# Performance work log

Measured on AMD Instinct MI355X. Metric: run time of the kernel, lower is better.

Reference implementation:

```python
import jax, jax.numpy as jnp
import numpy as np

EPS = 1e-12  # torch F.normalize eps


def setup_inputs() -> dict:
    key = jax.random.key(0)
    k1, k2, k3 = jax.random.split(key, 3)
    b, c, n, h, w = 8, 64, 8, 64, 64
    dims = 32
    x = jax.random.normal(k1, (b, c, n, h, w), dtype=jnp.float32)
    # 1x1 conv kernels collapse to [out_ch, in_ch] matrices
    w_q = jax.random.normal(k2, (dims, c), dtype=jnp.float32) * (1.0 / np.sqrt(c))
    w_kv = jax.random.normal(k3, (2 * dims, c), dtype=jnp.float32) * (1.0 / np.sqrt(c))
    return {"x": x, "w_q": w_q, "w_kv": w_kv}


def _l2norm(t, axis):
    nrm = jnp.sqrt(jnp.sum(t * t, axis=axis, keepdims=True))
    return t / jnp.maximum(nrm, EPS)


def reference(x, w_q, w_kv):
    b, c, n, h, w = x.shape
    d = w_q.shape[0]
    # spa_q: 1x1 stride-1 conv == channel GEMM -> [b, d, n, h, w]
    q = jnp.einsum('bcnhw,dc->bdnhw', x, w_q)
    x_s = x[:, :, :, ::2, ::2]                       # [b, c, n, h2, w2]
    kv = jnp.einsum('bcnhw,ec->benhw', x_s, w_kv)    # [b, 2d, n, h2, w2]
    k, v = kv[:, :d], kv[:, d:]
    h2, w2 = k.shape[-2], k.shape[-1]
    # unfold_q: b (h w) (d n)
    uq = q.transpose(0, 3, 4, 1, 2).reshape(b, h * w, d * n)
    # unfold_k: b (d n) (h2 w2)
    uk = k.reshape(b, d * n, h2 * w2)
    # unfold_v: b (h2 w2) (d n)
    uv = v.transpose(0, 3, 4, 1, 2).reshape(b, h2 * w2, d * n)
    uq = _l2norm(uq, axis=-1)
    uk = _l2norm(uk, axis=-2)
    att = jax.nn.softmax(jnp.einsum('bqf,bfk->bqk', uq, uk), axis=-1)
    out = jnp.einsum('bqk,bkf->bqf', att, uv)        # [b, h*w, d*n]
    # b (h w) (d n) -> b d n h w
    return out.reshape(b, h, w, d, n).transpose(0, 3, 4, 1, 2)
```

## Files before the change

kernel.cpp:

```cpp
#include <hip/hip_runtime.h>


typedef __attribute__((ext_vector_type(8))) short short8;
typedef __attribute__((ext_vector_type(4))) float floatx4;
typedef __attribute__((ext_vector_type(2))) unsigned uintx2;

__device__ __forceinline__ short f2bf(float f) {
    unsigned u = __builtin_bit_cast(unsigned, f);
    u += 0x7fffu + ((u >> 16) & 1u);
    return (short)(u >> 16);
}
__device__ __forceinline__ unsigned pack2bf(float a, float b) {
    return (unsigned)(unsigned short)f2bf(a) | ((unsigned)(unsigned short)f2bf(b) << 16);
}

__global__ __launch_bounds__(256) void proj(const float* __restrict__ x,
                                            const float* __restrict__ wq,
                                            const float* __restrict__ wkv,
                                            short* __restrict__ qraw,
                                            short* __restrict__ kraw,
                                            short* __restrict__ vraw) {
    int b = blockIdx.x >> 6, y = blockIdx.x & 63;
    int t = threadIdx.x;
    int n = t >> 5, dg = (t >> 3) & 3, xc = t & 7;
    bool kv = (y & 1) == 0;
    int y2 = y >> 1;

    __shared__ __align__(16) float wq_s[64 * 32];
    __shared__ __align__(16) float wkv_s[64 * 64];
    __shared__ __align__(16) float xs[128 * 36];
    __shared__ __align__(16) short k_lds[16 * 264];
    __shared__ __align__(16) short v_lds[256 * 16];
    __shared__ float red[32 * 33];
    __shared__ float nrm[32];
    short* q_lds = (short*)xs;

    for (int i = t; i < 2048; i += 256) { int d = i >> 6, c = i & 63; wq_s[c * 32 + d] = wq[i]; }
    for (int i = t; i < 4096; i += 256) { int e = i >> 6, c = i & 63; wkv_s[c * 64 + e] = wkv[i]; }
    const float* xb = x + (size_t)b * 2097152 + y * 64;

    for (int xh = 0; xh < 2; ++xh) {
        float qa[8][4], ka[8][2], va[8][2];
#pragma unroll
        for (int j = 0; j < 8; ++j) {
            qa[j][0] = qa[j][1] = qa[j][2] = qa[j][3] = 0.f;
            ka[j][0] = ka[j][1] = 0.f; va[j][0] = va[j][1] = 0.f;
        }
        for (int cc = 0; cc < 4; ++cc) {
            __syncthreads();
#pragma unroll
            for (int it = 0; it < 4; ++it) {
                int i = it * 256 + t, cn = i >> 3, e = i & 7;
                float4 v = *(const float4*)(xb + (size_t)(cc * 16 + (cn >> 3)) * 32768 + (cn & 7) * 4096 + xh * 32 + e * 4);
                *(float4*)(xs + cn * 36 + e * 4) = v;
            }
            __syncthreads();
            for (int c = 0; c < 16; ++c) {
                float4 xv = *(const float4*)(xs + (c * 8 + n) * 36 + xc * 4);
                float xw[4] = {xv.x, xv.y, xv.z, xv.w};
                int cg = cc * 16 + c;
                float4 wqa = *(const float4*)(wq_s + cg * 32 + dg * 8);
                float4 wqb = *(const float4*)(wq_s + cg * 32 + dg * 8 + 4);
                float wj[8] = {wqa.x, wqa.y, wqa.z, wqa.w, wqb.x, wqb.y, wqb.z, wqb.w};
#pragma unroll
                for (int j = 0; j < 8; ++j)
#pragma unroll
                    for (int i2 = 0; i2 < 4; ++i2) qa[j][i2] += wj[j] * xw[i2];
                if (kv) {
                    float4 wka = *(const float4*)(wkv_s + cg * 64 + dg * 8);
                    float4 wkb = *(const float4*)(wkv_s + cg * 64 + dg * 8 + 4);
                    float4 wva = *(const float4*)(wkv_s + cg * 64 + 32 + dg * 8);
                    float4 wvb = *(const float4*)(wkv_s + cg * 64 + 32 + dg * 8 + 4);
                    float wk[8] = {wka.x, wka.y, wka.z, wka.w, wkb.x, wkb.y, wkb.z, wkb.w};
                    float wv2[8] = {wva.x, wva.y, wva.z, wva.w, wvb.x, wvb.y, wvb.z, wvb.w};
#pragma unroll
                    for (int j = 0; j < 8; ++j) {
                        ka[j][0] += wk[j] * xw[0]; ka[j][1] += wk[j] * xw[2];
                        va[j][0] += wv2[j] * xw[0]; va[j][1] += wv2[j] * xw[2];
                    }
                }
            }
        }
        __syncthreads();
#pragma unroll
        for (int i2 = 0; i2 < 4; ++i2) {
            float s = 0.f;
#pragma unroll
            for (int j = 0; j < 8; ++j) s += qa[j][i2] * qa[j][i2];
            red[(xc * 4 + i2) * 33 + n * 4 + dg] = s;
        }
        __syncthreads();
        if (t < 32) {
            float s = 0.f;
            for (int k = 0; k < 32; ++k) s += red[t * 33 + k];
            nrm[t] = 1.f / fmaxf(sqrtf(s), 1e-12f);
        }
        __syncthreads();
#pragma unroll
        for (int i2 = 0; i2 < 4; ++i2) {
            float sc = nrm[xc * 4 + i2];
#pragma unroll
            for (int j = 0; j < 8; ++j)
                q_lds[(xc * 4 + i2) * 264 + (dg * 8 + j) * 8 + n] = f2bf(qa[j][i2] * sc);
        }
        __syncthreads();
        {
            size_t qg = ((size_t)b * 4096 + y * 64 + xh * 32) * 256;
#pragma unroll
            for (int it = 0; it < 4; ++it) {
                int r = it * 8 + (t >> 5), sg = t & 31;
                *(uint4*)(qraw + qg + (size_t)r * 256 + sg * 8) = *(const uint4*)(q_lds + r * 264 + sg * 8);
            }
        }
        if (kv) {
            __syncthreads();
#pragma unroll
            for (int ii = 0; ii < 2; ++ii) {
                float s = 0.f;
#pragma unroll
                for (int j = 0; j < 8; ++j) s += ka[j][ii] * ka[j][ii];
                red[(xc * 2 + ii) * 33 + n * 4 + dg] = s;
            }
            __syncthreads();
            if (t < 16) {
                float s = 0.f;
                for (int k = 0; k < 32; ++k) s += red[t * 33 + k];
                nrm[t] = 1.f / fmaxf(sqrtf(s), 1e-12f);
            }
            __syncthreads();
#pragma unroll
            for (int ii = 0; ii < 2; ++ii) {
                float sc = nrm[xc * 2 + ii];
#pragma unroll
                for (int j = 0; j < 8; ++j) {
                    int f = (dg * 8 + j) * 8 + n;
                    k_lds[(xc * 2 + ii) * 264 + f] = f2bf(ka[j][ii] * sc);
                    v_lds[f * 16 + xc * 2 + ii] = f2bf(va[j][ii]);
                }
            }
            __syncthreads();
            size_t kg = ((size_t)b * 1024 + y2 * 32 + xh * 16) * 256;
#pragma unroll
            for (int it = 0; it < 2; ++it) {
                int r = it * 8 + (t >> 5), sg = t & 31;
                *(uint4*)(kraw + kg + (size_t)r * 256 + sg * 8) = *(const uint4*)(k_lds + r * 264 + sg * 8);
            }
            size_t vg = (size_t)b * 262144 + (size_t)y2 * 32 + xh * 16;
#pragma unroll
            for (int it = 0; it < 2; ++it) {
                int idx = it * 256 + t, f = idx >> 1, hh = idx & 1;
                *(uint4*)(vraw + vg + (size_t)f * 1024 + hh * 8) = *(const uint4*)(v_lds + f * 16 + hh * 8);
            }
        }
    }
}

__global__ __launch_bounds__(256, 1) void attn(const short* __restrict__ qraw,
                                               const short* __restrict__ kraw,
                                               const short* __restrict__ vraw,
                                               float* __restrict__ out) {
    int b = blockIdx.x >> 5, qt = blockIdx.x & 31;
    int t = threadIdx.x, wv = t >> 6, lane = t & 63, l16 = lane & 15, quad = lane >> 4;

    __shared__ __align__(16) short k_s[2][32 * 264];
    __shared__ __align__(16) short v_s[2][256 * 40];
    __shared__ __align__(16) short p_s[2][128 * 40];
    __shared__ float dsum[128];

    short8 qf[2][8];
    const short* qb = qraw + ((size_t)b * 4096 + qt * 128 + wv * 32) * 256;
#pragma unroll
    for (int pt = 0; pt < 2; ++pt)
#pragma unroll
        for (int fs = 0; fs < 8; ++fs)
            qf[pt][fs] = *(const short8*)(qb + (pt * 16 + l16) * 256 + fs * 32 + quad * 8);

    floatx4 acc[8][4];
#pragma unroll
    for (int i = 0; i < 8; ++i)
#pragma unroll
        for (int j = 0; j < 4; ++j) acc[i][j] = (floatx4){0.f, 0.f, 0.f, 0.f};
    float dacc0 = 0.f, dacc1 = 0.f;

    int krow = t >> 3, kseg = t & 7;
    const short* kbase = kraw + ((size_t)b * 1024 + krow) * 256 + kseg * 32;
    const short* vbase = vraw + ((size_t)b * 256 + t) * 1024;

    short8 kst[4], vst[4];
#pragma unroll
    for (int j = 0; j < 4; ++j) {
        kst[j] = *(const short8*)(kbase + j * 8);
        vst[j] = *(const short8*)(vbase + j * 8);
    }
#pragma unroll
    for (int j = 0; j < 4; ++j) {
        *(short8*)(k_s[0] + krow * 264 + kseg * 32 + j * 8) = kst[j];
        *(short8*)(v_s[0] + t * 40 + j * 8) = vst[j];
    }
#pragma unroll
    for (int j = 0; j < 4; ++j) {
        kst[j] = *(const short8*)(kbase + (size_t)32 * 256 + j * 8);
        vst[j] = *(const short8*)(vbase + 32 + j * 8);
    }
    __syncthreads();

    for (int kc = 0; kc < 32; ++kc) {
        int cur = kc & 1, nxt = cur ^ 1;
        floatx4 cc0[2] = {(floatx4){0.f,0.f,0.f,0.f}, (floatx4){0.f,0.f,0.f,0.f}};
        floatx4 cc1[2] = {(floatx4){0.f,0.f,0.f,0.f}, (floatx4){0.f,0.f,0.f,0.f}};
#pragma unroll
        for (int kt = 0; kt < 2; ++kt) {
#pragma unroll
            for (int fs = 0; fs < 8; ++fs) {
                short8 a = *(const short8*)(k_s[cur] + (kt * 16 + l16) * 264 + fs * 32 + quad * 8);
                cc0[kt] = __builtin_amdgcn_mfma_f32_16x16x32_bf16(a, qf[0][fs], cc0[kt], 0, 0, 0);
                cc1[kt] = __builtin_amdgcn_mfma_f32_16x16x32_bf16(a, qf[1][fs], cc1[kt], 0, 0, 0);
            }
        }
#pragma unroll
        for (int kt = 0; kt < 2; ++kt) {
            float e0 = __expf(cc0[kt][0]), e1 = __expf(cc0[kt][1]);
            float e2 = __expf(cc0[kt][2]), e3 = __expf(cc0[kt][3]);
            dacc0 += (e0 + e1) + (e2 + e3);
            uintx2 w0; w0[0] = pack2bf(e0, e1); w0[1] = pack2bf(e2, e3);
            *(uintx2*)(p_s[cur] + (wv * 32 + l16) * 40 + kt * 16 + quad * 4) = w0;
            float f0 = __expf(cc1[kt][0]), f1 = __expf(cc1[kt][1]);
            float f2 = __expf(cc1[kt][2]), f3 = __expf(cc1[kt][3]);
            dacc1 += (f0 + f1) + (f2 + f3);
            uintx2 w1; w1[0] = pack2bf(f0, f1); w1[1] = pack2bf(f2, f3);
            *(uintx2*)(p_s[cur] + (wv * 32 + 16 + l16) * 40 + kt * 16 + quad * 4) = w1;
        }
        __syncthreads();

        if (kc < 31) {
#pragma unroll
            for (int j = 0; j < 4; ++j) {
                *(short8*)(k_s[nxt] + krow * 264 + kseg * 32 + j * 8) = kst[j];
                *(short8*)(v_s[nxt] + t * 40 + j * 8) = vst[j];
            }
        }
        short8 av[4];
#pragma unroll
        for (int fl = 0; fl < 4; ++fl)
            av[fl] = *(const short8*)(v_s[cur] + (wv * 64 + fl * 16 + l16) * 40 + quad * 8);
#pragma unroll
        for (int p2 = 0; p2 < 8; ++p2) {
            short8 bq = *(const short8*)(p_s[cur] + (p2 * 16 + l16) * 40 + quad * 8);
#pragma unroll
            for (int fl = 0; fl < 4; ++fl)
                acc[p2][fl] = __builtin_amdgcn_mfma_f32_16x16x32_bf16(av[fl], bq, acc[p2][fl], 0, 0, 0);
        }
        if (kc < 30) {
            int kp0n = (kc + 2) * 32;
#pragma unroll
            for (int j = 0; j < 4; ++j) {
                kst[j] = *(const short8*)(kbase + (size_t)kp0n * 256 + j * 8);
                vst[j] = *(const short8*)(vbase + kp0n + j * 8);
            }
        }
        __syncthreads();
    }
    dacc0 += __shfl_xor(dacc0, 16); dacc0 += __shfl_xor(dacc0, 32);
    dacc1 += __shfl_xor(dacc1, 16); dacc1 += __shfl_xor(dacc1, 32);
    if (quad == 0) {
        dsum[wv * 32 + l16] = dacc0;
        dsum[wv * 32 + 16 + l16] = dacc1;
    }
    __syncthreads();
    float* ob = out + (size_t)b * 1048576 + qt * 128;
#pragma unroll
    for (int p2 = 0; p2 < 8; ++p2) {
        float inv = 1.f / dsum[p2 * 16 + l16];
#pragma unroll
        for (int fl = 0; fl < 4; ++fl) {
            int f0 = wv * 64 + fl * 16 + quad * 4;
#pragma unroll
            for (int r = 0; r < 4; ++r)
                ob[(size_t)(f0 + r) * 4096 + p2 * 16 + l16] = acc[p2][fl][r] * inv;
        }
    }
}

extern "C" void kernel_launch(void* const* d_in, const int* in_sizes, int n_in,
                              void* d_out, int out_size, void* d_ws, size_t ws_size,
                              hipStream_t stream) {
    (void)in_sizes; (void)n_in; (void)out_size; (void)ws_size;
    const float* x   = (const float*)d_in[0];
    const float* wqp = (const float*)d_in[1];
    const float* wkv = (const float*)d_in[2];
    float* out = (float*)d_out;

    char* ws = (char*)d_ws;
    short* qraw = (short*)ws;
    short* kraw = (short*)(ws + 16777216);
    short* vraw = (short*)(ws + 16777216 + 4194304);

    proj<<<512, 256, 0, stream>>>(x, wqp, wkv, qraw, kraw, vraw);
    attn<<<256, 256, 0, stream>>>(qraw, kraw, vraw, out);
}
```

Measured before the change: 194.7 us.

## Split attention block across 8 waves with swizzled LDS and hardware bf16 pack

Doubles the attention block to 512 threads. The S=QK^T work is split by key half and the PV work is split by feature and query halves, so each wave holds half the accumulators. The two per-key-half denominator partials are combined at the end. K/V LDS stores and reads get an XOR swizzle to cut bank conflicts, the software bf16 rounding is replaced by v_cvt_pk_bf16_f32, and s_setprio is raised around MFMA loops. The aim is more waves per CU to hide latency and lower register pressure, at the cost of duplicated Q fragment loads and more threads per barrier.

```diff
diff --git a/kernel.cpp b/kernel.cpp
--- a/kernel.cpp
+++ b/kernel.cpp
@@ -10,8 +10,11 @@
     u += 0x7fffu + ((u >> 16) & 1u);
     return (short)(u >> 16);
 }
-__device__ __forceinline__ unsigned pack2bf(float a, float b) {
-    return (unsigned)(unsigned short)f2bf(a) | ((unsigned)(unsigned short)f2bf(b) << 16);
+
+__device__ __forceinline__ unsigned cvtpk_bf16(float lo, float hi) {
+    unsigned r;
+    asm("v_cvt_pk_bf16_f32 %0, %1, %2" : "=v"(r) : "v"(lo), "v"(hi));
+    return r;
 }
 
 __global__ __launch_bounds__(256) void proj(const float* __restrict__ x,
@@ -155,7 +158,7 @@
     }
 }
 
-__global__ __launch_bounds__(256, 1) void attn(const short* __restrict__ qraw,
+__global__ __launch_bounds__(512, 2) void attn(const short* __restrict__ qraw,
                                                const short* __restrict__ kraw,
                                                const short* __restrict__ vraw,
                                                float* __restrict__ out) {
@@ -165,97 +168,104 @@
     __shared__ __align__(16) short k_s[2][32 * 264];
     __shared__ __align__(16) short v_s[2][256 * 40];
     __shared__ __align__(16) short p_s[2][128 * 40];
-    __shared__ float dsum[128];
+    __shared__ float dsum[2][128];
+
+    int kt = wv & 1, pp = wv >> 1;
+    int fh = wv & 3, ph = wv >> 2;
 
     short8 qf[2][8];
-    const short* qb = qraw + ((size_t)b * 4096 + qt * 128 + wv * 32) * 256;
+    const short* qb = qraw + ((size_t)b * 4096 + qt * 128 + pp * 32) * 256;
 #pragma unroll
     for (int pt = 0; pt < 2; ++pt)
 #pragma unroll
         for (int fs = 0; fs < 8; ++fs)
             qf[pt][fs] = *(const short8*)(qb + (pt * 16 + l16) * 256 + fs * 32 + quad * 8);
 
-    floatx4 acc[8][4];
-#pragma unroll
-    for (int i = 0; i < 8; ++i)
+    floatx4 acc[4][4];
+#pragma unroll
+    for (int i = 0; i < 4; ++i)
 #pragma unroll
         for (int j = 0; j < 4; ++j) acc[i][j] = (floatx4){0.f, 0.f, 0.f, 0.f};
     float dacc0 = 0.f, dacc1 = 0.f;
 
-    int krow = t >> 3, kseg = t & 7;
-    const short* kbase = kraw + ((size_t)b * 1024 + krow) * 256 + kseg * 32;
-    const short* vbase = vraw + ((size_t)b * 256 + t) * 1024;
-
-    short8 kst[4], vst[4];
-#pragma unroll
-    for (int j = 0; j < 4; ++j) {
+    int krow = t >> 4, kseg = t & 15;
+    int vrow = t >> 1, vhalf = t & 1;
+    int sk = (kseg >> 2) & 1, sv = (t >> 4) & 1;
+    const short* kbase = kraw + ((size_t)b * 1024 + krow) * 256 + kseg * 16;
+    const short* vbase = vraw + ((size_t)b * 256 + vrow) * 1024 + vhalf * 16;
+
+    short8 kst[2], vst[2];
+#pragma unroll
+    for (int j = 0; j < 2; ++j) {
         kst[j] = *(const short8*)(kbase + j * 8);
         vst[j] = *(const short8*)(vbase + j * 8);
     }
 #pragma unroll
-    for (int j = 0; j < 4; ++j) {
-        *(short8*)(k_s[0] + krow * 264 + kseg * 32 + j * 8) = kst[j];
-        *(short8*)(v_s[0] + t * 40 + j * 8) = vst[j];
-    }
-#pragma unroll
-    for (int j = 0; j < 4; ++j) {
-        kst[j] = *(const short8*)(kbase + (size_t)32 * 256 + j * 8);
+    for (int j = 0; j < 2; ++j) {
+        *(short8*)(k_s[0] + krow * 264 + kseg * 16 + (j ^ sk) * 8) = kst[j];
+        *(short8*)(v_s[0] + vrow * 40 + vhalf * 16 + (j ^ sv) * 8) = vst[j];
+    }
+#pragma unroll
+    for (int j = 0; j < 2; ++j) {
+        kst[j] = *(const short8*)(kbase + 8192 + j * 8);
         vst[j] = *(const short8*)(vbase + 32 + j * 8);
     }
     __syncthreads();
 
+    int s2 = (l16 >> 3) & 1;
     for (int kc = 0; kc < 32; ++kc) {
         int cur = kc & 1, nxt = cur ^ 1;
-        floatx4 cc0[2] = {(floatx4){0.f,0.f,0.f,0.f}, (floatx4){0.f,0.f,0.f,0.f}};
-        floatx4 cc1[2] = {(floatx4){0.f,0.f,0.f,0.f}, (floatx4){0.f,0.f,0.f,0.f}};
-#pragma unroll
-        for (int kt = 0; kt < 2; ++kt) {
-#pragma unroll
-            for (int fs = 0; fs < 8; ++fs) {
-                short8 a = *(const short8*)(k_s[cur] + (kt * 16 + l16) * 264 + fs * 32 + quad * 8);
-                cc0[kt] = __builtin_amdgcn_mfma_f32_16x16x32_bf16(a, qf[0][fs], cc0[kt], 0, 0, 0);
-                cc1[kt] = __builtin_amdgcn_mfma_f32_16x16x32_bf16(a, qf[1][fs], cc1[kt], 0, 0, 0);
-            }
-        }
-#pragma unroll
-        for (int kt = 0; kt < 2; ++kt) {
-            float e0 = __expf(cc0[kt][0]), e1 = __expf(cc0[kt][1]);
-            float e2 = __expf(cc0[kt][2]), e3 = __expf(cc0[kt][3]);
+        floatx4 cc0 = (floatx4){0.f, 0.f, 0.f, 0.f};
+        floatx4 cc1 = (floatx4){0.f, 0.f, 0.f, 0.f};
+        const short* krd = k_s[cur] + (kt * 16 + l16) * 264;
+        __builtin_amdgcn_s_setprio(1);
+#pragma unroll
+        for (int fs = 0; fs < 8; ++fs) {
+            short8 a = *(const short8*)(krd + fs * 32 + (quad ^ ((fs >> 1) & 1)) * 8);
+            cc0 = __builtin_amdgcn_mfma_f32_16x16x32_bf16(a, qf[0][fs], cc0, 0, 0, 0);
+            cc1 = __builtin_amdgcn_mfma_f32_16x16x32_bf16(a, qf[1][fs], cc1, 0, 0, 0);
+        }
+        __builtin_amdgcn_s_setprio(0);
+        {
+            float e0 = __expf(cc0[0]), e1 = __expf(cc0[1]);
+            float e2 = __expf(cc0[2]), e3 = __expf(cc0[3]);
             dacc0 += (e0 + e1) + (e2 + e3);
-            uintx2 w0; w0[0] = pack2bf(e0, e1); w0[1] = pack2bf(e2, e3);
-            *(uintx2*)(p_s[cur] + (wv * 32 + l16) * 40 + kt * 16 + quad * 4) = w0;
-            float f0 = __expf(cc1[kt][0]), f1 = __expf(cc1[kt][1]);
-            float f2 = __expf(cc1[kt][2]), f3 = __expf(cc1[kt][3]);
+            uintx2 w0; w0[0] = cvtpk_bf16(e0, e1); w0[1] = cvtpk_bf16(e2, e3);
+            *(uintx2*)(p_s[cur] + (pp * 32 + l16) * 40 + kt * 16 + quad * 4) = w0;
+            float f0 = __expf(cc1[0]), f1 = __expf(cc1[1]);
+            float f2 = __expf(cc1[2]), f3 = __expf(cc1[3]);
             dacc1 += (f0 + f1) + (f2 + f3);
-            uintx2 w1; w1[0] = pack2bf(f0, f1); w1[1] = pack2bf(f2, f3);
-            *(uintx2*)(p_s[cur] + (wv * 32 + 16 + l16) * 40 + kt * 16 + quad * 4) = w1;
+            uintx2 w1; w1[0] = cvtpk_bf16(f0, f1); w1[1] = cvtpk_bf16(f2, f3);
+            *(uintx2*)(p_s[cur] + (pp * 32 + 16 + l16) * 40 + kt * 16 + quad * 4) = w1;
         }
         __syncthreads();
 
         if (kc < 31) {
 #pragma unroll
-            for (int j = 0; j < 4; ++j) {
-                *(short8*)(k_s[nxt] + krow * 264 + kseg * 32 + j * 8) = kst[j];
-                *(short8*)(v_s[nxt] + t * 40 + j * 8) = vst[j];
+            for (int j = 0; j < 2; ++j) {
+                *(short8*)(k_s[nxt] + krow * 264 + kseg * 16 + (j ^ sk) * 8) = kst[j];
+                *(short8*)(v_s[nxt] + vrow * 40 + vhalf * 16 + (j ^ sv) * 8) = vst[j];
             }
         }
         short8 av[4];
 #pragma unroll
         for (int fl = 0; fl < 4; ++fl)
-            av[fl] = *(const short8*)(v_s[cur] + (wv * 64 + fl * 16 + l16) * 40 + quad * 8);
-#pragma unroll
-        for (int p2 = 0; p2 < 8; ++p2) {
-            short8 bq = *(const short8*)(p_s[cur] + (p2 * 16 + l16) * 40 + quad * 8);
+            av[fl] = *(const short8*)(v_s[cur] + (fh * 64 + fl * 16 + l16) * 40 + (quad ^ s2) * 8);
+        __builtin_amdgcn_s_setprio(1);
+#pragma unroll
+        for (int p2 = 0; p2 < 4; ++p2) {
+            short8 bq = *(const short8*)(p_s[cur] + (ph * 64 + p2 * 16 + l16) * 40 + quad * 8);
 #pragma unroll
             for (int fl = 0; fl < 4; ++fl)
                 acc[p2][fl] = __builtin_amdgcn_mfma_f32_16x16x32_bf16(av[fl], bq, acc[p2][fl], 0, 0, 0);
         }
+        __builtin_amdgcn_s_setprio(0);
         if (kc < 30) {
-            int kp0n = (kc + 2) * 32;
-#pragma unroll
-            for (int j = 0; j < 4; ++j) {
-                kst[j] = *(const short8*)(kbase + (size_t)kp0n * 256 + j * 8);
-                vst[j] = *(const short8*)(vbase + kp0n + j * 8);
+            int koff = (kc + 2) * 8192, voff = (kc + 2) * 32;
+#pragma unroll
+            for (int j = 0; j < 2; ++j) {
+                kst[j] = *(const short8*)(kbase + koff + j * 8);
+                vst[j] = *(const short8*)(vbase + voff + j * 8);
             }
         }
         __syncthreads();
@@ -263,20 +273,21 @@
     dacc0 += __shfl_xor(dacc0, 16); dacc0 += __shfl_xor(dacc0, 32);
     dacc1 += __shfl_xor(dacc1, 16); dacc1 += __shfl_xor(dacc1, 32);
     if (quad == 0) {
-        dsum[wv * 32 + l16] = dacc0;
-        dsum[wv * 32 + 16 + l16] = dacc1;
+        dsum[kt][pp * 32 + l16] = dacc0;
+        dsum[kt][pp * 32 + 16 + l16] = dacc1;
     }
     __syncthreads();
     float* ob = out + (size_t)b * 1048576 + qt * 128;
 #pragma unroll
-    for (int p2 = 0; p2 < 8; ++p2) {
-        float inv = 1.f / dsum[p2 * 16 + l16];
+    for (int p2 = 0; p2 < 4; ++p2) {
+        int pcol = ph * 64 + p2 * 16 + l16;
+        float inv = 1.f / (dsum[0][pcol] + dsum[1][pcol]);
 #pragma unroll
         for (int fl = 0; fl < 4; ++fl) {
-            int f0 = wv * 64 + fl * 16 + quad * 4;
+            int f0 = fh * 64 + fl * 16 + quad * 4;
 #pragma unroll
             for (int r = 0; r < 4; ++r)
-                ob[(size_t)(f0 + r) * 4096 + p2 * 16 + l16] = acc[p2][fl][r] * inv;
+                ob[(size_t)(f0 + r) * 4096 + pcol] = acc[p2][fl][r] * inv;
         }
     }
 }
@@ -296,5 +307,5 @@
     short* vraw = (short*)(ws + 16777216 + 4194304);
 
     proj<<<512, 256, 0, stream>>>(x, wqp, wkv, qraw, kraw, vraw);
-    attn<<<256, 256, 0, stream>>>(qraw, kraw, vraw, out);
-}
+    attn<<<256, 512, 0, stream>>>(qraw, kraw, vraw, out);
+}
```

Result: faster. 184.0 us (-5.5%).
